# Performance work log

Measured on AMD Instinct MI355X. Metric: run time of the kernel, lower is better.

Reference implementation:

```python
import jax, jax.numpy as jnp
import numpy as np

EMBED_DIM = 1024
NUM_HEADS = 16
HEAD_DIM = EMBED_DIM // NUM_HEADS


def setup_inputs() -> dict:
    key = jax.random.key(0)
    ks = jax.random.split(key, 7)
    N, L = 2, 2048
    sv = 1.0 / np.sqrt(HEAD_DIM)
    so = 1.0 / np.sqrt(EMBED_DIM)
    return {
        "values": jax.random.normal(ks[0], (N, L, EMBED_DIM), jnp.float32),
        "keys": jax.random.normal(ks[1], (N, L, EMBED_DIM), jnp.float32),
        "query": jax.random.normal(ks[2], (N, L, EMBED_DIM), jnp.float32),
        # NOTE: original torch code applies self.values to v, k AND q; keys/queries
        # Linears are dead parameters, so only Wv/bv and fc_out are materialized.
        "Wv": jax.random.uniform(ks[3], (HEAD_DIM, HEAD_DIM), jnp.float32, -sv, sv),
        "bv": jax.random.uniform(ks[4], (HEAD_DIM,), jnp.float32, -sv, sv),
        "Wo": jax.random.uniform(ks[5], (EMBED_DIM, EMBED_DIM), jnp.float32, -so, so),
        "bo": jax.random.uniform(ks[6], (EMBED_DIM,), jnp.float32, -so, so),
    }


def reference(values, keys, query, Wv, bv, Wo, bo):
    N, Lq, _ = query.shape
    Lk = keys.shape[1]
    Lv = values.shape[1]
    # split heads: (N, L, H, D)
    v = values.reshape(N, Lv, NUM_HEADS, HEAD_DIM)
    k = keys.reshape(N, Lk, NUM_HEADS, HEAD_DIM)
    q = query.reshape(N, Lq, NUM_HEADS, HEAD_DIM)
    # faithful to source: the SAME value projection is applied to v, k, q
    proj = lambda x: jnp.einsum('nlhd,ed->nlhe', x, Wv) + bv
    v = proj(v)
    k = proj(k)
    q = proj(q)
    # energy: (N, H, Q, K); note scaling by sqrt(embed_dim), as in source
    energy = jnp.einsum('nqhd,nkhd->nhqk', q, k)
    attention = jax.nn.softmax(energy / jnp.sqrt(jnp.float32(EMBED_DIM)), axis=3)
    out = jnp.einsum('nhql,nlhd->nqhd', attention, v).reshape(N, Lq, EMBED_DIM)
    return out @ Wo.T + bo
```

## Files before the change

kernel.cpp:

```cpp
#include <hip/hip_runtime.h>

typedef unsigned short u16;
typedef __bf16 bf16x4 __attribute__((ext_vector_type(4)));
typedef __bf16 bf16x8 __attribute__((ext_vector_type(8)));
typedef float  f32x4  __attribute__((ext_vector_type(4)));

#define MFMA16(a, b, c) __builtin_amdgcn_mfma_f32_16x16x32_bf16((a), (b), (c), 0, 0, 0)


__global__ __launch_bounds__(256) void conv_wo_kernel(const float* __restrict__ Wo,
                                                      u16* __restrict__ Wob) {
    const int i = (blockIdx.x * 256 + threadIdx.x) * 4;
    float4 v = *(const float4*)&Wo[i];
    bf16x4 o = { (__bf16)v.x, (__bf16)v.y, (__bf16)v.z, (__bf16)v.w };
    *(bf16x4*)&Wob[i] = o;
}

__global__ __launch_bounds__(256) void proj_kernel(
    const float* __restrict__ values, const float* __restrict__ keys,
    const float* __restrict__ query,  const float* __restrict__ Wv,
    const float* __restrict__ bv,
    u16* __restrict__ Qb, u16* __restrict__ Kb, u16* __restrict__ VTb) {
    __shared__ __align__(16) u16 Wvs[64 * 72];
    __shared__ __align__(16) u16 Xs[64 * 72];
    const int b = blockIdx.x;
    const int lt = b & 31, h = (b >> 5) & 15, n = (b >> 9) & 1, t = b >> 10;
    const int nh = n * 16 + h, l0 = lt * 64;
    const int tid = threadIdx.x, wave = tid >> 6, lane = tid & 63;
    const int quad = lane >> 4, l16 = lane & 15;
    const float* xin = (t == 0) ? values : (t == 1 ? keys : query);

#pragma unroll
    for (int j = 0; j < 4; ++j) {
        const int chunk = tid + 256 * j, r = chunk >> 4, c = (chunk & 15) * 4;
        float4 w = *(const float4*)&Wv[r * 64 + c];
        bf16x4 wb = { (__bf16)w.x, (__bf16)w.y, (__bf16)w.z, (__bf16)w.w };
        *(bf16x4*)&Wvs[r * 72 + c] = wb;
        float4 x = *(const float4*)&xin[(size_t)(n * 2048 + l0 + r) * 1024 + h * 64 + c];
        bf16x4 xb = { (__bf16)x.x, (__bf16)x.y, (__bf16)x.z, (__bf16)x.w };
        *(bf16x4*)&Xs[r * 72 + c] = xb;
    }
    __syncthreads();

    bf16x8 wf[4][2], xf[2];
#pragma unroll
    for (int f = 0; f < 4; ++f)
#pragma unroll
        for (int ks = 0; ks < 2; ++ks)
            wf[f][ks] = *(const bf16x8*)&Wvs[(f * 16 + l16) * 72 + ks * 32 + quad * 8];
#pragma unroll
    for (int ks = 0; ks < 2; ++ks)
        xf[ks] = *(const bf16x8*)&Xs[(wave * 16 + l16) * 72 + ks * 32 + quad * 8];

    f32x4 acc[4];
#pragma unroll
    for (int i = 0; i < 4; ++i) acc[i] = (f32x4){0.f, 0.f, 0.f, 0.f};

    if (t == 0) {
#pragma unroll
        for (int nf = 0; nf < 4; ++nf) {
            acc[nf] = MFMA16(xf[0], wf[nf][0], acc[nf]);
            acc[nf] = MFMA16(xf[1], wf[nf][1], acc[nf]);
        }
    } else {
#pragma unroll
        for (int mf = 0; mf < 4; ++mf) {
            acc[mf] = MFMA16(wf[mf][0], xf[0], acc[mf]);
            acc[mf] = MFMA16(wf[mf][1], xf[1], acc[mf]);
        }
    }
    __syncthreads();

    const float scale = (t == 2) ? 0.04508422f : 1.0f;
    if (t == 0) {
#pragma unroll
        for (int nf = 0; nf < 4; ++nf) {
            const float bias = bv[nf * 16 + l16];
            bf16x4 o = { (__bf16)(acc[nf][0] + bias), (__bf16)(acc[nf][1] + bias),
                         (__bf16)(acc[nf][2] + bias), (__bf16)(acc[nf][3] + bias) };
            *(bf16x4*)&Xs[(nf * 16 + l16) * 72 + wave * 16 + quad * 4] = o;
        }
    } else {
#pragma unroll
        for (int mf = 0; mf < 4; ++mf) {
            bf16x4 o = { (__bf16)((acc[mf][0] + bv[mf * 16 + quad * 4 + 0]) * scale),
                         (__bf16)((acc[mf][1] + bv[mf * 16 + quad * 4 + 1]) * scale),
                         (__bf16)((acc[mf][2] + bv[mf * 16 + quad * 4 + 2]) * scale),
                         (__bf16)((acc[mf][3] + bv[mf * 16 + quad * 4 + 3]) * scale) };
            *(bf16x4*)&Xs[(wave * 16 + l16) * 72 + mf * 16 + quad * 4] = o;
        }
    }
    __syncthreads();

    u16* dst = (t == 0) ? VTb : (t == 1 ? Kb : Qb);
#pragma unroll
    for (int j = 0; j < 2; ++j) {
        const int chunk = tid + 256 * j, r = chunk >> 3, c = (chunk & 7) * 8;
        const size_t off = (t == 0) ? (size_t)(nh * 64 + r) * 2048 + l0 + c
                                    : (size_t)(nh * 2048 + l0 + r) * 64 + c;
        *(int4*)&dst[off] = *(const int4*)&Xs[r * 72 + c];
    }
}

__global__ __launch_bounds__(512) void flash_kernel(
    const u16* __restrict__ Qb, const u16* __restrict__ Kb,
    const u16* __restrict__ VTb, u16* __restrict__ AOb) {
    __shared__ __align__(16) u16 Ks[64 * 72];
    __shared__ __align__(16) u16 Vs[64 * 72];
    __shared__ __align__(16) u16 Ps[8][16 * 72];
    const int b = blockIdx.x, nh = b >> 4, qb = b & 15;
    const int tid = threadIdx.x, wave = tid >> 6, lane = tid & 63;
    const int quad = lane >> 4, l16 = lane & 15;
    const int q0 = qb * 128 + wave * 16;
    const u16* Qg = Qb + ((size_t)nh * 2048 + q0) * 64;
    u16* Pw = &Ps[wave][0];

#pragma unroll
    for (int j = 0; j < 2; ++j) {
        const int chunk = lane + 64 * j, r = chunk >> 3, c = (chunk & 7) * 8;
        *(int4*)&Pw[r * 72 + c] = *(const int4*)&Qg[r * 64 + c];
    }
    bf16x8 qf[2];
#pragma unroll
    for (int ks = 0; ks < 2; ++ks)
        qf[ks] = *(const bf16x8*)&Pw[l16 * 72 + ks * 32 + quad * 8];

    f32x4 Ot[4];
#pragma unroll
    for (int i = 0; i < 4; ++i) Ot[i] = (f32x4){0.f, 0.f, 0.f, 0.f};
    float lsum = 0.f;

    const u16* Kg = Kb + (size_t)nh * 2048 * 64;
    const u16* Vg = VTb + (size_t)nh * 64 * 2048;

    for (int kt = 0; kt < 32; ++kt) {
        __syncthreads();
        const int k0 = kt * 64;
        {
            const int r = tid >> 3, c = (tid & 7) * 8;
            *(int4*)&Ks[r * 72 + c] = *(const int4*)&Kg[(size_t)(k0 + r) * 64 + c];
            *(int4*)&Vs[r * 72 + c] = *(const int4*)&Vg[(size_t)r * 2048 + k0 + c];
        }
        __syncthreads();

#pragma unroll
        for (int mf = 0; mf < 4; ++mf) {
            bf16x8 ak0 = *(const bf16x8*)&Ks[(mf * 16 + l16) * 72 + quad * 8];
            bf16x8 ak1 = *(const bf16x8*)&Ks[(mf * 16 + l16) * 72 + 32 + quad * 8];
            f32x4 s = (f32x4){0.f, 0.f, 0.f, 0.f};
            s = MFMA16(ak0, qf[0], s);
            s = MFMA16(ak1, qf[1], s);
            const float p0 = __builtin_amdgcn_exp2f(s[0]);
            const float p1 = __builtin_amdgcn_exp2f(s[1]);
            const float p2 = __builtin_amdgcn_exp2f(s[2]);
            const float p3 = __builtin_amdgcn_exp2f(s[3]);
            lsum += (p0 + p1) + (p2 + p3);
            bf16x4 pk = { (__bf16)p0, (__bf16)p1, (__bf16)p2, (__bf16)p3 };
            *(bf16x4*)&Pw[l16 * 72 + mf * 16 + quad * 4] = pk;
        }

#pragma unroll
        for (int ks = 0; ks < 2; ++ks) {
            bf16x8 bp = *(const bf16x8*)&Pw[l16 * 72 + ks * 32 + quad * 8];
#pragma unroll
            for (int md = 0; md < 4; ++md) {
                bf16x8 av = *(const bf16x8*)&Vs[(md * 16 + l16) * 72 + ks * 32 + quad * 8];
                Ot[md] = MFMA16(av, bp, Ot[md]);
            }
        }
    }

    float s = lsum;
    s += __shfl_xor(s, 16);
    s += __shfl_xor(s, 32);
    const float linv = 1.0f / s;

#pragma unroll
    for (int md = 0; md < 4; ++md) {
        bf16x4 o = { (__bf16)(Ot[md][0] * linv), (__bf16)(Ot[md][1] * linv),
                     (__bf16)(Ot[md][2] * linv), (__bf16)(Ot[md][3] * linv) };
        *(bf16x4*)&Pw[l16 * 72 + md * 16 + quad * 4] = o;
    }
    u16* dstb = AOb + ((size_t)(nh >> 4) * 2048 + q0) * 1024 + (nh & 15) * 64;
#pragma unroll
    for (int j = 0; j < 2; ++j) {
        const int chunk = lane + 64 * j, r = chunk >> 3, c = (chunk & 7) * 8;
        *(int4*)&dstb[(size_t)r * 1024 + c] = *(const int4*)&Pw[r * 72 + c];
    }
}

__global__ __launch_bounds__(256) void out_gemm_kernel(
    const u16* __restrict__ A, const u16* __restrict__ Bw,
    const float* __restrict__ bo, float* __restrict__ out) {
    __shared__ __align__(16) u16 As[64 * 72];
    __shared__ __align__(16) u16 Bs[64 * 72];
    const int b = blockIdx.x, rt = b >> 4, ct = b & 15;
    const int row0 = rt * 64, col0 = ct * 64;
    const int tid = threadIdx.x, wave = tid >> 6, lane = tid & 63;
    const int quad = lane >> 4, l16 = lane & 15;

    f32x4 acc[4];
#pragma unroll
    for (int i = 0; i < 4; ++i) acc[i] = (f32x4){0.f, 0.f, 0.f, 0.f};

    for (int kt = 0; kt < 16; ++kt) {
        __syncthreads();
        const int k0 = kt * 64;
#pragma unroll
        for (int j = 0; j < 2; ++j) {
            const int chunk = tid + 256 * j, r = chunk >> 3, c = (chunk & 7) * 8;
            *(int4*)&As[r * 72 + c] = *(const int4*)&A[(size_t)(row0 + r) * 1024 + k0 + c];
            *(int4*)&Bs[r * 72 + c] = *(const int4*)&Bw[(size_t)(col0 + r) * 1024 + k0 + c];
        }
        __syncthreads();
#pragma unroll
        for (int ks = 0; ks < 2; ++ks) {
            bf16x8 af = *(const bf16x8*)&As[(wave * 16 + l16) * 72 + ks * 32 + quad * 8];
#pragma unroll
            for (int fc = 0; fc < 4; ++fc) {
                bf16x8 bfr = *(const bf16x8*)&Bs[(fc * 16 + l16) * 72 + ks * 32 + quad * 8];
                acc[fc] = MFMA16(af, bfr, acc[fc]);
            }
        }
    }

#pragma unroll
    for (int fc = 0; fc < 4; ++fc) {
        const float bias = bo[col0 + fc * 16 + l16];
        const int row = row0 + wave * 16 + quad * 4;
        const int col = col0 + fc * 16 + l16;
#pragma unroll
        for (int r = 0; r < 4; ++r)
            out[(size_t)(row + r) * 1024 + col] = acc[fc][r] + bias;
    }
}

extern "C" void kernel_launch(void* const* d_in, const int* in_sizes, int n_in,
                              void* d_out, int out_size, void* d_ws, size_t ws_size,
                              hipStream_t stream) {
    (void)in_sizes; (void)n_in; (void)out_size; (void)ws_size;
    const float* values = (const float*)d_in[0];
    const float* keys   = (const float*)d_in[1];
    const float* query  = (const float*)d_in[2];
    const float* Wv     = (const float*)d_in[3];
    const float* bv     = (const float*)d_in[4];
    const float* Wo     = (const float*)d_in[5];
    const float* bo     = (const float*)d_in[6];

    char* ws = (char*)d_ws;
    u16* Qb  = (u16*)(ws);
    u16* Kb  = (u16*)(ws + (8ull  << 20));
    u16* VTb = (u16*)(ws + (16ull << 20));
    u16* AOb = (u16*)(ws + (24ull << 20));
    u16* Wob = (u16*)(ws + (32ull << 20));

    conv_wo_kernel<<<1024, 256, 0, stream>>>(Wo, Wob);
    proj_kernel<<<3072, 256, 0, stream>>>(values, keys, query, Wv, bv, Qb, Kb, VTb);
    flash_kernel<<<512, 512, 0, stream>>>(Qb, Kb, VTb, AOb);
    out_gemm_kernel<<<1024, 256, 0, stream>>>(AOb, Wob, bo, (float*)d_out);
}
```

Measured before the change: 196.9 us.

## Split attention over key halves with 32x32 MFMA tiles and a combine kernel

The flash kernel now uses 32x32x16 MFMA tiles, so each wave handles 32 queries instead of 16. The key range is split into two halves across blocks, giving 1024 blocks of 256 threads. Each block writes fp32 partial outputs and row sums, and a new combine kernel adds the two halves, normalises, and writes bf16 to the attention output. This is meant to raise occupancy and MFMA efficiency, at the cost of an extra launch and the fp32 partial-result traffic to global memory.

```diff
diff --git a/kernel.cpp b/kernel.cpp
--- a/kernel.cpp
+++ b/kernel.cpp
@@ -4,8 +4,10 @@
 typedef __bf16 bf16x4 __attribute__((ext_vector_type(4)));
 typedef __bf16 bf16x8 __attribute__((ext_vector_type(8)));
 typedef float  f32x4  __attribute__((ext_vector_type(4)));
+typedef float  f32x16 __attribute__((ext_vector_type(16)));
 
 #define MFMA16(a, b, c) __builtin_amdgcn_mfma_f32_16x16x32_bf16((a), (b), (c), 0, 0, 0)
+#define MFMA32(a, b, c) __builtin_amdgcn_mfma_f32_32x32x16_bf16((a), (b), (c), 0, 0, 0)
 
 
 __global__ __launch_bounds__(256) void conv_wo_kernel(const float* __restrict__ Wo,
@@ -102,91 +104,113 @@
     }
 }
 
-__global__ __launch_bounds__(512) void flash_kernel(
+__global__ __launch_bounds__(256, 4) void flash_kernel(
     const u16* __restrict__ Qb, const u16* __restrict__ Kb,
-    const u16* __restrict__ VTb, u16* __restrict__ AOb) {
+    const u16* __restrict__ VTb, float* __restrict__ Opart,
+    float* __restrict__ Lp) {
     __shared__ __align__(16) u16 Ks[64 * 72];
     __shared__ __align__(16) u16 Vs[64 * 72];
-    __shared__ __align__(16) u16 Ps[8][16 * 72];
-    const int b = blockIdx.x, nh = b >> 4, qb = b & 15;
+    __shared__ __align__(16) u16 Ps[4][32 * 72];
+    const int b = blockIdx.x;
+    const int nh = b >> 5, qsl = (b >> 1) & 15, ks = b & 1;
     const int tid = threadIdx.x, wave = tid >> 6, lane = tid & 63;
-    const int quad = lane >> 4, l16 = lane & 15;
-    const int q0 = qb * 128 + wave * 16;
+    const int l32 = lane & 31, half = lane >> 5;
+    const int q0 = qsl * 128 + wave * 32;
+    const int s4 = (b >> 1) * 4 + wave;
+    u16* Pw = &Ps[wave][0];
+
     const u16* Qg = Qb + ((size_t)nh * 2048 + q0) * 64;
-    u16* Pw = &Ps[wave][0];
-
-#pragma unroll
-    for (int j = 0; j < 2; ++j) {
-        const int chunk = lane + 64 * j, r = chunk >> 3, c = (chunk & 7) * 8;
-        *(int4*)&Pw[r * 72 + c] = *(const int4*)&Qg[r * 64 + c];
-    }
-    bf16x8 qf[2];
-#pragma unroll
-    for (int ks = 0; ks < 2; ++ks)
-        qf[ks] = *(const bf16x8*)&Pw[l16 * 72 + ks * 32 + quad * 8];
-
-    f32x4 Ot[4];
-#pragma unroll
-    for (int i = 0; i < 4; ++i) Ot[i] = (f32x4){0.f, 0.f, 0.f, 0.f};
+    bf16x8 qf[4];
+#pragma unroll
+    for (int kg = 0; kg < 4; ++kg)
+        qf[kg] = *(const bf16x8*)&Qg[l32 * 64 + kg * 16 + half * 8];
+
+    f32x16 Oacc[2];
+#pragma unroll
+    for (int dt = 0; dt < 2; ++dt)
+#pragma unroll
+        for (int r = 0; r < 16; ++r) Oacc[dt][r] = 0.f;
     float lsum = 0.f;
 
     const u16* Kg = Kb + (size_t)nh * 2048 * 64;
     const u16* Vg = VTb + (size_t)nh * 64 * 2048;
 
-    for (int kt = 0; kt < 32; ++kt) {
-        __syncthreads();
-        const int k0 = kt * 64;
-        {
-            const int r = tid >> 3, c = (tid & 7) * 8;
+    for (int kt = 0; kt < 16; ++kt) {
+        __syncthreads();
+        const int k0 = ks * 1024 + kt * 64;
+#pragma unroll
+        for (int j = 0; j < 2; ++j) {
+            const int chunk = tid + 256 * j, r = chunk >> 3, c = (chunk & 7) * 8;
             *(int4*)&Ks[r * 72 + c] = *(const int4*)&Kg[(size_t)(k0 + r) * 64 + c];
             *(int4*)&Vs[r * 72 + c] = *(const int4*)&Vg[(size_t)r * 2048 + k0 + c];
         }
         __syncthreads();
 
 #pragma unroll
-        for (int mf = 0; mf < 4; ++mf) {
-            bf16x8 ak0 = *(const bf16x8*)&Ks[(mf * 16 + l16) * 72 + quad * 8];
-            bf16x8 ak1 = *(const bf16x8*)&Ks[(mf * 16 + l16) * 72 + 32 + quad * 8];
-            f32x4 s = (f32x4){0.f, 0.f, 0.f, 0.f};
-            s = MFMA16(ak0, qf[0], s);
-            s = MFMA16(ak1, qf[1], s);
-            const float p0 = __builtin_amdgcn_exp2f(s[0]);
-            const float p1 = __builtin_amdgcn_exp2f(s[1]);
-            const float p2 = __builtin_amdgcn_exp2f(s[2]);
-            const float p3 = __builtin_amdgcn_exp2f(s[3]);
-            lsum += (p0 + p1) + (p2 + p3);
-            bf16x4 pk = { (__bf16)p0, (__bf16)p1, (__bf16)p2, (__bf16)p3 };
-            *(bf16x4*)&Pw[l16 * 72 + mf * 16 + quad * 4] = pk;
-        }
-
-#pragma unroll
-        for (int ks = 0; ks < 2; ++ks) {
-            bf16x8 bp = *(const bf16x8*)&Pw[l16 * 72 + ks * 32 + quad * 8];
-#pragma unroll
-            for (int md = 0; md < 4; ++md) {
-                bf16x8 av = *(const bf16x8*)&Vs[(md * 16 + l16) * 72 + ks * 32 + quad * 8];
-                Ot[md] = MFMA16(av, bp, Ot[md]);
-            }
-        }
-    }
-
-    float s = lsum;
-    s += __shfl_xor(s, 16);
-    s += __shfl_xor(s, 32);
-    const float linv = 1.0f / s;
-
-#pragma unroll
-    for (int md = 0; md < 4; ++md) {
-        bf16x4 o = { (__bf16)(Ot[md][0] * linv), (__bf16)(Ot[md][1] * linv),
-                     (__bf16)(Ot[md][2] * linv), (__bf16)(Ot[md][3] * linv) };
-        *(bf16x4*)&Pw[l16 * 72 + md * 16 + quad * 4] = o;
-    }
-    u16* dstb = AOb + ((size_t)(nh >> 4) * 2048 + q0) * 1024 + (nh & 15) * 64;
-#pragma unroll
-    for (int j = 0; j < 2; ++j) {
-        const int chunk = lane + 64 * j, r = chunk >> 3, c = (chunk & 7) * 8;
-        *(int4*)&dstb[(size_t)r * 1024 + c] = *(const int4*)&Pw[r * 72 + c];
-    }
+        for (int t2 = 0; t2 < 2; ++t2) {
+            f32x16 s;
+#pragma unroll
+            for (int r = 0; r < 16; ++r) s[r] = 0.f;
+#pragma unroll
+            for (int kg = 0; kg < 4; ++kg) {
+                bf16x8 ak = *(const bf16x8*)&Ks[(t2 * 32 + l32) * 72 + kg * 16 + half * 8];
+                s = MFMA32(ak, qf[kg], s);
+            }
+#pragma unroll
+            for (int a = 0; a < 4; ++a) {
+                const float p0 = __builtin_amdgcn_exp2f(s[4 * a + 0]);
+                const float p1 = __builtin_amdgcn_exp2f(s[4 * a + 1]);
+                const float p2 = __builtin_amdgcn_exp2f(s[4 * a + 2]);
+                const float p3 = __builtin_amdgcn_exp2f(s[4 * a + 3]);
+                lsum += (p0 + p1) + (p2 + p3);
+                bf16x4 pk = { (__bf16)p0, (__bf16)p1, (__bf16)p2, (__bf16)p3 };
+                *(bf16x4*)&Pw[l32 * 72 + t2 * 32 + a * 8 + half * 4] = pk;
+            }
+        }
+
+#pragma unroll
+        for (int kk = 0; kk < 4; ++kk) {
+            bf16x8 bp = *(const bf16x8*)&Pw[l32 * 72 + kk * 16 + half * 8];
+#pragma unroll
+            for (int dt = 0; dt < 2; ++dt) {
+                bf16x8 av = *(const bf16x8*)&Vs[(dt * 32 + l32) * 72 + kk * 16 + half * 8];
+                Oacc[dt] = MFMA32(av, bp, Oacc[dt]);
+            }
+        }
+    }
+
+    float* Ob = Opart + ((size_t)s4 * 2 + ks) * 2048;
+#pragma unroll
+    for (int dt = 0; dt < 2; ++dt)
+#pragma unroll
+        for (int r = 0; r < 16; ++r)
+            Ob[(dt * 16 + r) * 64 + lane] = Oacc[dt][r];
+    Lp[((size_t)s4 * 2 + ks) * 64 + lane] = lsum;
+}
+
+__global__ __launch_bounds__(256) void combine_kernel(
+    const float* __restrict__ Opart, const float* __restrict__ Lp,
+    u16* __restrict__ AOb) {
+    const int s4 = blockIdx.x;
+    const int nh = s4 >> 6, qsl = (s4 >> 2) & 15, w = s4 & 3;
+    const int t = threadIdx.x, q = t >> 3, dg = t & 7;
+    const int dt = dg >> 2, a = dg & 3;
+
+    const size_t b0 = (size_t)s4 * 2 * 2048;
+    const float ls = Lp[(size_t)s4 * 2 * 64 + q] + Lp[(size_t)s4 * 2 * 64 + 32 + q]
+                   + Lp[((size_t)s4 * 2 + 1) * 64 + q] + Lp[((size_t)s4 * 2 + 1) * 64 + 32 + q];
+    const float inv = 1.0f / ls;
+
+    bf16x8 o;
+#pragma unroll
+    for (int i = 0; i < 8; ++i) {
+        const int r = 4 * a + (i & 3), hf = i >> 2;
+        const size_t off = (size_t)(dt * 16 + r) * 64 + hf * 32 + q;
+        o[i] = (__bf16)((Opart[b0 + off] + Opart[b0 + 2048 + off]) * inv);
+    }
+    const int row = (nh >> 4) * 2048 + qsl * 128 + w * 32 + q;
+    const int col = (nh & 15) * 64 + dg * 8;
+    *(bf16x8*)&AOb[(size_t)row * 1024 + col] = o;
 }
 
 __global__ __launch_bounds__(256) void out_gemm_kernel(
@@ -248,14 +272,17 @@
     const float* bo     = (const float*)d_in[6];
 
     char* ws = (char*)d_ws;
-    u16* Qb  = (u16*)(ws);
-    u16* Kb  = (u16*)(ws + (8ull  << 20));
-    u16* VTb = (u16*)(ws + (16ull << 20));
-    u16* AOb = (u16*)(ws + (24ull << 20));
-    u16* Wob = (u16*)(ws + (32ull << 20));
+    u16*   Qb    = (u16*)(ws);
+    u16*   Kb    = (u16*)(ws + (8ull  << 20));
+    u16*   VTb   = (u16*)(ws + (16ull << 20));
+    u16*   AOb   = (u16*)(ws + (24ull << 20));
+    u16*   Wob   = (u16*)(ws + (32ull << 20));
+    float* Opart = (float*)(ws + (34ull << 20));
+    float* Lp    = (float*)(ws + (66ull << 20));
 
     conv_wo_kernel<<<1024, 256, 0, stream>>>(Wo, Wob);
     proj_kernel<<<3072, 256, 0, stream>>>(values, keys, query, Wv, bv, Qb, Kb, VTb);
-    flash_kernel<<<512, 512, 0, stream>>>(Qb, Kb, VTb, AOb);
+    flash_kernel<<<1024, 256, 0, stream>>>(Qb, Kb, VTb, Opart, Lp);
+    combine_kernel<<<2048, 256, 0, stream>>>(Opart, Lp, AOb);
     out_gemm_kernel<<<1024, 256, 0, stream>>>(AOb, Wob, bo, (float*)d_out);
 }
```

Result: faster. 191.7 us (-2.7%).
